# Optimization experiments

Measured on AMD Instinct MI355X. Metric: run time of the kernel, lower is better.

The kernel has to match this reference:

```python
import jax, jax.numpy as jnp
import numpy as np

B, ACT, C, H = 2048, 14, 128, 32
N = B * ACT                      # total nodes
E = B * ACT * ACT                # batched GCN edges
LOG_STD_MIN, LOG_STD_MAX = -20.0, 2.0


def setup_inputs() -> dict:
    key = jax.random.key(0)
    ks = jax.random.split(key, 8)
    def w(k, shape, fan_in):
        return jax.random.normal(k, shape, jnp.float32) / np.sqrt(fan_in).astype(np.float32)
    return {
        "state": jax.random.normal(ks[0], (N, C), jnp.float32),
        "conv_W": w(ks[1], (C, C), C),
        "conv_b": jnp.zeros((C,), jnp.float32),
        "lin1_W": w(ks[2], (2 * C, H), 2 * C),
        "lin1_b": jnp.zeros((H,), jnp.float32),
        "lin2_W": w(ks[3], (H, H), H),
        "lin2_b": jnp.zeros((H,), jnp.float32),
        "mu_W": w(ks[4], (H, 1), H),
        "mu_b": jnp.zeros((1,), jnp.float32),
        "sig_W": w(ks[5], (H, 1), H),
        "sig_b": jnp.zeros((1,), jnp.float32),
        "edge_index": jax.random.randint(ks[6], (2, E), 0, N, jnp.int32),
    }


def gcn_conv(x, W, b, src, dst):
    # PyG GCNConv default: add self-loops + symmetric normalization
    xw = x @ W                                           # [N, C]
    ones = jnp.ones(src.shape, x.dtype)
    deg = jax.ops.segment_sum(ones, dst, num_segments=N) + 1.0   # self-loop included
    dinv = jax.lax.rsqrt(deg)                            # deg^{-1/2}
    norm = dinv[src] * dinv[dst]                         # per-edge weight
    agg = jax.ops.segment_sum(xw[src] * norm[:, None], dst, num_segments=N)
    return agg + xw * (dinv * dinv)[:, None] + b         # self-loop term + bias


def reference(state, conv_W, conv_b, lin1_W, lin1_b, lin2_W, lin2_b,
              mu_W, mu_b, sig_W, sig_b, edge_index):
    src, dst = edge_index[0], edge_index[1]
    out = jax.nn.relu(gcn_conv(state, conv_W, conv_b, src, dst))
    x = (out + state).reshape(B, ACT, C)                 # [B, 14, C]
    # self.edges = all 196 directed pairs (i, j) over the 14-node graph
    e_src = jnp.repeat(jnp.arange(ACT), ACT)             # edges[:, 0]
    e_dst = jnp.tile(jnp.arange(ACT), ACT)               # edges[:, 1]
    ef = jnp.concatenate([x[:, e_src, :], x[:, e_dst, :]], axis=2)  # [B, 196, 2C]
    h = jax.nn.leaky_relu(ef @ lin1_W + lin1_b)          # slope 0.01 (torch default)
    h = jax.nn.leaky_relu(h @ lin2_W + lin2_b)           # [B, 196, H]
    log_std = jnp.clip(h @ sig_W + sig_b, LOG_STD_MIN, LOG_STD_MAX)
    std = jnp.exp(log_std)[..., 0]                       # [B, 196]
    mu = jax.nn.softplus(h @ mu_W + mu_b + 1e-10)[..., 0]  # [B, 196]
    # distribution parameters (return_D / deterministic paths)
    return jnp.stack([mu, std], axis=0)                  # [2, B, 196]
```

## Files before the change

### kernel.cpp

```cpp
#include <hip/hip_runtime.h>
#include <hip/hip_bf16.h>
#include <math.h>

#define NB    2048
#define ACT   14
#define NC    128
#define NH    32
#define NNODE (NB*ACT)
#define NEDGE (NB*ACT*ACT)
#define NPAIR (NB*ACT*ACT)
#define BCAP  64

typedef __attribute__((ext_vector_type(8))) short bf16x8;
typedef __attribute__((ext_vector_type(4))) float f32x4;

__device__ __forceinline__ unsigned short f2bf(float f)
{
    unsigned u = __float_as_uint(f);
    return (unsigned short)((u + 0x7fff + ((u >> 16) & 1)) >> 16);
}
__device__ __forceinline__ float bf2f(unsigned short h)
{
    return __uint_as_float(((unsigned)h) << 16);
}
__device__ __forceinline__ float bfl(unsigned v) { return __uint_as_float(v << 16); }
__device__ __forceinline__ float bfh(unsigned v) { return __uint_as_float(v & 0xffff0000u); }

__global__ __launch_bounds__(256) void init_misc(
    int* __restrict__ cnt, unsigned short* __restrict__ ydummy,
    const float* __restrict__ convW, unsigned short* __restrict__ convWt,
    const float* __restrict__ W1,
    unsigned short* __restrict__ Whi, unsigned short* __restrict__ Wlo)
{
    int idx = blockIdx.x * 256 + threadIdx.x;
    if (idx < NNODE) cnt[idx] = 0;
    if (idx < 128) ydummy[idx] = 0;
    if (idx < 128 * 128) {
        int c = idx >> 7, k = idx & 127;
        convWt[idx] = f2bf(convW[k * 128 + c]);
    }
    if (idx < 64 * 128) {
        int c = idx >> 7, k = idx & 127;
        float w = (c < 32) ? W1[k * 32 + c] : W1[(128 + k) * 32 + (c - 32)];
        unsigned short h = f2bf(w);
        Whi[idx] = h;
        Wlo[idx] = f2bf(w - bf2f(h));
    }
}

__global__ void bucket_fill(const int* __restrict__ src, const int* __restrict__ dst,
                            int* __restrict__ cnt, int* __restrict__ bucket)
{
    int e = blockIdx.x * blockDim.x + threadIdx.x;
    if (e < NEDGE) {
        int d = dst[e];
        int slot = atomicAdd(&cnt[d], 1);
        if (slot < BCAP) bucket[(size_t)d * BCAP + slot] = src[e];
    }
}

__global__ __launch_bounds__(256) void gemm1_mfma(
    const float* __restrict__ A, const unsigned short* __restrict__ Bt,
    const int* __restrict__ cnt, unsigned short* __restrict__ y)
{
    __shared__ unsigned short Ah[128 * 128];
    __shared__ unsigned short Alo[128 * 128];
    __shared__ unsigned short Bl[128 * 128];
    const int tid  = threadIdx.x;
    const int row0 = blockIdx.x * 128;

#pragma unroll
    for (int it = 0; it < 16; ++it) {
        int idx = tid + it * 256;
        int r = idx >> 5;
        int c = (idx & 31) << 2;
        float4 v = ((const float4*)(A + (size_t)(row0 + r) * 128))[idx & 31];
        ushort4 h, l;
        h.x = f2bf(v.x); l.x = f2bf(v.x - bf2f(h.x));
        h.y = f2bf(v.y); l.y = f2bf(v.y - bf2f(h.y));
        h.z = f2bf(v.z); l.z = f2bf(v.z - bf2f(h.z));
        h.w = f2bf(v.w); l.w = f2bf(v.w - bf2f(h.w));
        int byte = (r * 256 + c * 2) ^ ((r & 7) << 4);
        *(ushort4*)((char*)Ah  + byte) = h;
        *(ushort4*)((char*)Alo + byte) = l;
    }
#pragma unroll
    for (int it = 0; it < 8; ++it) {
        int idx = tid + it * 256;
        int cc = idx >> 4;
        int kk = (idx & 15) << 3;
        bf16x8 v = *((const bf16x8*)(Bt + cc * 128 + kk));
        int byte = (cc * 256 + kk * 2) ^ ((cc & 7) << 4);
        *(bf16x8*)((char*)Bl + byte) = v;
    }
    __syncthreads();

    const int wv = tid >> 6, lane = tid & 63;
    const int lr = lane & 15, kb = lane >> 4;
    const int col0 = wv * 32;

    f32x4 acc0[8], acc1[8];
#pragma unroll
    for (int mt = 0; mt < 8; ++mt) {
        acc0[mt] = (f32x4){0.f, 0.f, 0.f, 0.f};
        acc1[mt] = (f32x4){0.f, 0.f, 0.f, 0.f};
    }

#pragma unroll
    for (int ks = 0; ks < 4; ++ks) {
        const int kbyte = (ks * 32 + kb * 8) * 2;
        int cb0 = ((col0 + lr) * 256 + kbyte) ^ (((col0 + lr) & 7) << 4);
        int cb1 = ((col0 + 16 + lr) * 256 + kbyte) ^ (((col0 + 16 + lr) & 7) << 4);
        bf16x8 b0 = *(const bf16x8*)((char*)Bl + cb0);
        bf16x8 b1 = *(const bf16x8*)((char*)Bl + cb1);
#pragma unroll
        for (int mt = 0; mt < 8; ++mt) {
            int rr = mt * 16 + lr;
            int ab = (rr * 256 + kbyte) ^ ((rr & 7) << 4);
            bf16x8 ah = *(const bf16x8*)((char*)Ah  + ab);
            bf16x8 al = *(const bf16x8*)((char*)Alo + ab);
            acc0[mt] = __builtin_amdgcn_mfma_f32_16x16x32_bf16(ah, b0, acc0[mt], 0, 0, 0);
            acc0[mt] = __builtin_amdgcn_mfma_f32_16x16x32_bf16(al, b0, acc0[mt], 0, 0, 0);
            acc1[mt] = __builtin_amdgcn_mfma_f32_16x16x32_bf16(ah, b1, acc1[mt], 0, 0, 0);
            acc1[mt] = __builtin_amdgcn_mfma_f32_16x16x32_bf16(al, b1, acc1[mt], 0, 0, 0);
        }
    }

#pragma unroll
    for (int mt = 0; mt < 8; ++mt) {
#pragma unroll
        for (int t = 0; t < 4; ++t) {
            int grow = row0 + mt * 16 + kb * 4 + t;
            float s = rsqrtf((float)cnt[grow] + 1.0f);
            y[(size_t)grow * 128 + col0 + lr]      = f2bf(acc0[mt][t] * s);
            y[(size_t)grow * 128 + col0 + 16 + lr] = f2bf(acc1[mt][t] * s);
        }
    }
}

__global__ __launch_bounds__(256) void gemm2_mfma(
    const float* __restrict__ X, const unsigned short* __restrict__ Whi,
    const unsigned short* __restrict__ Wlo, float* __restrict__ U)
{
    __shared__ unsigned short Ah[64 * 128];
    __shared__ unsigned short Alo[64 * 128];
    __shared__ unsigned short Bh[64 * 128];
    __shared__ unsigned short Blo[64 * 128];
    const int tid  = threadIdx.x;
    const int row0 = blockIdx.x * 64;

#pragma unroll
    for (int it = 0; it < 8; ++it) {
        int idx = tid + it * 256;
        int r = idx >> 5;
        int c = (idx & 31) << 2;
        float4 v = ((const float4*)(X + (size_t)(row0 + r) * 128))[idx & 31];
        ushort4 h, l;
        h.x = f2bf(v.x); l.x = f2bf(v.x - bf2f(h.x));
        h.y = f2bf(v.y); l.y = f2bf(v.y - bf2f(h.y));
        h.z = f2bf(v.z); l.z = f2bf(v.z - bf2f(h.z));
        h.w = f2bf(v.w); l.w = f2bf(v.w - bf2f(h.w));
        int byte = (r * 256 + c * 2) ^ ((r & 7) << 4);
        *(ushort4*)((char*)Ah  + byte) = h;
        *(ushort4*)((char*)Alo + byte) = l;
    }
#pragma unroll
    for (int it = 0; it < 4; ++it) {
        int idx = tid + it * 256;
        int cc = idx >> 4;
        int kk = (idx & 15) << 3;
        int byte = (cc * 256 + kk * 2) ^ ((cc & 7) << 4);
        *(bf16x8*)((char*)Bh  + byte) = *((const bf16x8*)(Whi + cc * 128 + kk));
        *(bf16x8*)((char*)Blo + byte) = *((const bf16x8*)(Wlo + cc * 128 + kk));
    }
    __syncthreads();

    const int wv = tid >> 6, lane = tid & 63;
    const int lr = lane & 15, kb = lane >> 4;
    const int col0 = wv * 16;

    f32x4 acc[4];
#pragma unroll
    for (int mt = 0; mt < 4; ++mt) acc[mt] = (f32x4){0.f, 0.f, 0.f, 0.f};

#pragma unroll
    for (int ks = 0; ks < 4; ++ks) {
        const int kbyte = (ks * 32 + kb * 8) * 2;
        int cb = ((col0 + lr) * 256 + kbyte) ^ (((col0 + lr) & 7) << 4);
        bf16x8 bh = *(const bf16x8*)((char*)Bh  + cb);
        bf16x8 bl = *(const bf16x8*)((char*)Blo + cb);
#pragma unroll
        for (int mt = 0; mt < 4; ++mt) {
            int rr = mt * 16 + lr;
            int ab = (rr * 256 + kbyte) ^ ((rr & 7) << 4);
            bf16x8 ah = *(const bf16x8*)((char*)Ah  + ab);
            bf16x8 al = *(const bf16x8*)((char*)Alo + ab);
            acc[mt] = __builtin_amdgcn_mfma_f32_16x16x32_bf16(ah, bh, acc[mt], 0, 0, 0);
            acc[mt] = __builtin_amdgcn_mfma_f32_16x16x32_bf16(al, bh, acc[mt], 0, 0, 0);
            acc[mt] = __builtin_amdgcn_mfma_f32_16x16x32_bf16(ah, bl, acc[mt], 0, 0, 0);
        }
    }

#pragma unroll
    for (int mt = 0; mt < 4; ++mt) {
#pragma unroll
        for (int t = 0; t < 4; ++t) {
            int grow = row0 + mt * 16 + kb * 4 + t;
            U[(size_t)grow * 64 + col0 + lr] = acc[mt][t];
        }
    }
}

__global__ __launch_bounds__(256) void gather_agg(
    const int* __restrict__ bucket, const int* __restrict__ cnt,
    const unsigned short* __restrict__ y, const float* __restrict__ bias,
    const float* __restrict__ state, float* __restrict__ xout)
{
    const int lane = threadIdx.x & 31;
    const int d = (blockIdx.x * 256 + threadIdx.x) >> 5;
    if (d >= NNODE) return;

    const int c_true = cnt[d];
    const int c = c_true < BCAP ? c_true : BCAP;

    uint2 sv0 = ((const uint2*)(y + (size_t)d * NC))[lane];
    float4 acc;
    acc.x = bfl(sv0.x); acc.y = bfh(sv0.x);
    acc.z = bfl(sv0.y); acc.w = bfh(sv0.y);

    const int* brow = bucket + (size_t)d * BCAP;
    for (int base = 0; base < c; base += 32) {
        int rem = c - base;
        int m = rem < 32 ? rem : 32;
        int sv = (lane < m) ? brow[base + lane] : NNODE;
        int mm = (m + 3) & ~3;
        for (int j = 0; j < mm; j += 4) {
            int s0 = __shfl(sv, j + 0, 32);
            int s1 = __shfl(sv, j + 1, 32);
            int s2 = __shfl(sv, j + 2, 32);
            int s3 = __shfl(sv, j + 3, 32);
            uint2 a0 = ((const uint2*)(y + (size_t)s0 * NC))[lane];
            uint2 a1 = ((const uint2*)(y + (size_t)s1 * NC))[lane];
            uint2 a2 = ((const uint2*)(y + (size_t)s2 * NC))[lane];
            uint2 a3 = ((const uint2*)(y + (size_t)s3 * NC))[lane];
            acc.x += bfl(a0.x) + bfl(a1.x) + bfl(a2.x) + bfl(a3.x);
            acc.y += bfh(a0.x) + bfh(a1.x) + bfh(a2.x) + bfh(a3.x);
            acc.z += bfl(a0.y) + bfl(a1.y) + bfl(a2.y) + bfl(a3.y);
            acc.w += bfh(a0.y) + bfh(a1.y) + bfh(a2.y) + bfh(a3.y);
        }
    }

    const float dv = rsqrtf((float)c_true + 1.0f);
    float4 b  = ((const float4*)bias)[lane];
    float4 st = ((const float4*)(state + (size_t)d * NC))[lane];
    float4 r;
    r.x = fmaxf(acc.x * dv + b.x, 0.f) + st.x;
    r.y = fmaxf(acc.y * dv + b.y, 0.f) + st.y;
    r.z = fmaxf(acc.z * dv + b.z, 0.f) + st.z;
    r.w = fmaxf(acc.w * dv + b.w, 0.f) + st.w;
    ((float4*)(xout + (size_t)d * NC))[lane] = r;
}

__device__ __forceinline__ float softplusf(float z)
{
    return z > 0.f ? z + log1pf(expf(-z)) : log1pf(expf(z));
}

__global__ __launch_bounds__(256) void pairs_lds_kernel(
    const float* __restrict__ uv, const float* __restrict__ W2,
    const float* __restrict__ b1, const float* __restrict__ b2,
    const float* __restrict__ muW, const float* __restrict__ mu_b,
    const float* __restrict__ sigW, const float* __restrict__ sig_b,
    float* __restrict__ out)
{
    __shared__ float uvs[42 * 68];
    const int tid = threadIdx.x;
    const int b0 = (blockIdx.x * 256) / 196;
    const int nodebase = b0 * ACT;

#pragma unroll
    for (int it = 0; it < 3; ++it) {
        int c = tid + it * 256;
        if (c < 42 * 16) {
            int r = c >> 4, q = c & 15;
            if (nodebase + r < NNODE) {
                float4 v = ((const float4*)(uv + (size_t)(nodebase + r) * 64))[q];
                *((float4*)&uvs[r * 68 + q * 4]) = v;
            }
        }
    }
    __syncthreads();

    const int gid = blockIdx.x * 256 + tid;
    const int b = gid / 196;
    const int p = gid - b * 196;
    const int i = p / 14;
    const int j = p - i * 14;

    const float* up = uvs + ((b - b0) * ACT + i) * 68;
    const float* vp = uvs + ((b - b0) * ACT + j) * 68 + 32;

    float h2[32];
#pragma unroll
    for (int l = 0; l < 32; ++l) h2[l] = b2[l];

#pragma unroll 2
    for (int k4 = 0; k4 < 8; ++k4) {
        float4 uu = *((const float4*)(up + k4 * 4));
        float4 vv = *((const float4*)(vp + k4 * 4));
#pragma unroll
        for (int kk = 0; kk < 4; ++kk) {
            float uvk = (kk == 0) ? uu.x + vv.x :
                        (kk == 1) ? uu.y + vv.y :
                        (kk == 2) ? uu.z + vv.z : uu.w + vv.w;
            float z = uvk + b1[k4 * 4 + kk];
            float h1k = z > 0.f ? z : 0.01f * z;
            const float* wrow = W2 + (k4 * 4 + kk) * 32;
#pragma unroll
            for (int l = 0; l < 32; ++l)
                h2[l] += h1k * wrow[l];
        }
    }

    float mu_acc = mu_b[0] + 1e-10f;
    float sg = sig_b[0];
#pragma unroll
    for (int l = 0; l < 32; ++l) {
        float h = h2[l];
        h = h > 0.f ? h : 0.01f * h;
        mu_acc += h * muW[l];
        sg += h * sigW[l];
    }
    out[gid]         = softplusf(mu_acc);
    out[NPAIR + gid] = expf(fminf(fmaxf(sg, -20.f), 2.f));
}

extern "C" void kernel_launch(void* const* d_in, const int* in_sizes, int n_in,
                              void* d_out, int out_size, void* d_ws, size_t ws_size,
                              hipStream_t stream)
{
    const float* state  = (const float*)d_in[0];
    const float* conv_W = (const float*)d_in[1];
    const float* conv_b = (const float*)d_in[2];
    const float* lin1_W = (const float*)d_in[3];
    const float* lin1_b = (const float*)d_in[4];
    const float* lin2_W = (const float*)d_in[5];
    const float* lin2_b = (const float*)d_in[6];
    const float* mu_W   = (const float*)d_in[7];
    const float* mu_b   = (const float*)d_in[8];
    const float* sig_W  = (const float*)d_in[9];
    const float* sig_b  = (const float*)d_in[10];
    const int*   eidx   = (const int*)d_in[11];
    const int* e_src = eidx;
    const int* e_dst = eidx + NEDGE;

    float* out = (float*)d_out;

    char* wsb = (char*)d_ws;
    unsigned short* y = (unsigned short*)wsb;
    char* p = wsb + (size_t)(NNODE + 1) * NC * sizeof(unsigned short);
    float* x = (float*)p;            p += (size_t)NNODE * NC * sizeof(float);
    int* cnt = (int*)p;              p += (size_t)NNODE * sizeof(int);
    int* bucket = (int*)p;           p += (size_t)NNODE * BCAP * sizeof(int);
    unsigned short* convWt = (unsigned short*)p;  p += 128 * 128 * sizeof(unsigned short);
    unsigned short* Whi = (unsigned short*)p;     p += 64 * 128 * sizeof(unsigned short);
    unsigned short* Wlo = (unsigned short*)p;     p += 64 * 128 * sizeof(unsigned short);
    float* uvb = (float*)p;

    init_misc<<<(NNODE + 255) / 256, 256, 0, stream>>>(
        cnt, y + (size_t)NNODE * NC, conv_W, convWt, lin1_W, Whi, Wlo);

    bucket_fill<<<NEDGE / 256, 256, 0, stream>>>(e_src, e_dst, cnt, bucket);

    gemm1_mfma<<<NNODE / 128, 256, 0, stream>>>(state, convWt, cnt, y);

    gather_agg<<<(NNODE * 32) / 256, 256, 0, stream>>>(
        bucket, cnt, y, conv_b, state, x);

    gemm2_mfma<<<NNODE / 64, 256, 0, stream>>>(x, Whi, Wlo, uvb);

    pairs_lds_kernel<<<NPAIR / 256, 256, 0, stream>>>(
        uvb, lin2_W, lin1_b, lin2_b, mu_W, mu_b, sig_W, sig_b, out);
}
```

Before: 83.00 us.

## Compute pair-MLP second layer with bf16 MFMA instead of scalar FMA

The per-pair 32x32 lin2 matmul, previously a scalar FMA loop per thread, now runs on the matrix cores via mfma_f32_16x16x32_bf16. lin2_W is pre-transposed into a bf16 column-major buffer during init, and each wave handles 4 tiles of 16 pairs. Results are staged through shared memory so each thread can finish the mu/sigma heads for its own pair. This cuts the large FMA count and register pressure, but adds bf16 rounding on h1 and W2, plus extra LDS traffic and shared memory per block.

Result: faster. 76.93 us (-7.3%).

```diff
diff --git a/kernel.cpp b/kernel.cpp
--- a/kernel.cpp
+++ b/kernel.cpp
@@ -30,7 +30,8 @@
     int* __restrict__ cnt, unsigned short* __restrict__ ydummy,
     const float* __restrict__ convW, unsigned short* __restrict__ convWt,
     const float* __restrict__ W1,
-    unsigned short* __restrict__ Whi, unsigned short* __restrict__ Wlo)
+    unsigned short* __restrict__ Whi, unsigned short* __restrict__ Wlo,
+    const float* __restrict__ W2, unsigned short* __restrict__ W2cm)
 {
     int idx = blockIdx.x * 256 + threadIdx.x;
     if (idx < NNODE) cnt[idx] = 0;
@@ -45,6 +46,10 @@
         unsigned short h = f2bf(w);
         Whi[idx] = h;
         Wlo[idx] = f2bf(w - bf2f(h));
+    }
+    if (idx < 1024) {
+        int c = idx >> 5, kk = idx & 31;
+        W2cm[c * 32 + kk] = f2bf(W2[kk * 32 + c]);
     }
 }
 
@@ -265,16 +270,26 @@
 {
     return z > 0.f ? z + log1pf(expf(-z)) : log1pf(expf(z));
 }
-
-__global__ __launch_bounds__(256) void pairs_lds_kernel(
-    const float* __restrict__ uv, const float* __restrict__ W2,
+__device__ __forceinline__ float leakyf(float z)
+{
+    return z > 0.f ? z : 0.01f * z;
+}
+
+__global__ __launch_bounds__(256) void pairs_mfma5_kernel(
+    const float* __restrict__ uv, const unsigned short* __restrict__ W2cm,
     const float* __restrict__ b1, const float* __restrict__ b2,
     const float* __restrict__ muW, const float* __restrict__ mu_b,
     const float* __restrict__ sigW, const float* __restrict__ sig_b,
     float* __restrict__ out)
 {
     __shared__ float uvs[42 * 68];
-    const int tid = threadIdx.x;
+    __shared__ float h2s[4][64 * 33];
+    const int tid  = threadIdx.x;
+    const int wv   = tid >> 6;
+    const int lane = tid & 63;
+    const int lr   = lane & 15;
+    const int kb   = lane >> 4;
+    const int k0   = kb * 8;
     const int b0 = (blockIdx.x * 256) / 196;
     const int nodebase = b0 * ACT;
 
@@ -289,50 +304,63 @@
             }
         }
     }
+    bf16x8 bfr0 = *((const bf16x8*)(W2cm + (size_t)lr * 32 + k0));
+    bf16x8 bfr1 = *((const bf16x8*)(W2cm + (size_t)(16 + lr) * 32 + k0));
+    float4 c0 = *((const float4*)(b1 + k0));
+    float4 c1 = *((const float4*)(b1 + k0 + 4));
     __syncthreads();
 
-    const int gid = blockIdx.x * 256 + tid;
-    const int b = gid / 196;
-    const int p = gid - b * 196;
-    const int i = p / 14;
-    const int j = p - i * 14;
-
-    const float* up = uvs + ((b - b0) * ACT + i) * 68;
-    const float* vp = uvs + ((b - b0) * ACT + j) * 68 + 32;
-
-    float h2[32];
-#pragma unroll
-    for (int l = 0; l < 32; ++l) h2[l] = b2[l];
-
-#pragma unroll 2
-    for (int k4 = 0; k4 < 8; ++k4) {
-        float4 uu = *((const float4*)(up + k4 * 4));
-        float4 vv = *((const float4*)(vp + k4 * 4));
-#pragma unroll
-        for (int kk = 0; kk < 4; ++kk) {
-            float uvk = (kk == 0) ? uu.x + vv.x :
-                        (kk == 1) ? uu.y + vv.y :
-                        (kk == 2) ? uu.z + vv.z : uu.w + vv.w;
-            float z = uvk + b1[k4 * 4 + kk];
-            float h1k = z > 0.f ? z : 0.01f * z;
-            const float* wrow = W2 + (k4 * 4 + kk) * 32;
-#pragma unroll
-            for (int l = 0; l < 32; ++l)
-                h2[l] += h1k * wrow[l];
+    float* h2w = h2s[wv];
+#pragma unroll
+    for (int tt = 0; tt < 4; ++tt) {
+        const int g = blockIdx.x * 256 + wv * 64 + tt * 16 + lr;
+        const int b = g / 196;
+        const int p = g - b * 196;
+        const int i = p / 14;
+        const int j = p - i * 14;
+        const float* up = &uvs[((b - b0) * ACT + i) * 68 + k0];
+        const float* vp = &uvs[((b - b0) * ACT + j) * 68 + 32 + k0];
+        float4 u0 = *((const float4*)up);
+        float4 u1 = *((const float4*)(up + 4));
+        float4 v0 = *((const float4*)vp);
+        float4 v1 = *((const float4*)(vp + 4));
+
+        bf16x8 a;
+        a[0] = (short)f2bf(leakyf(u0.x + v0.x + c0.x));
+        a[1] = (short)f2bf(leakyf(u0.y + v0.y + c0.y));
+        a[2] = (short)f2bf(leakyf(u0.z + v0.z + c0.z));
+        a[3] = (short)f2bf(leakyf(u0.w + v0.w + c0.w));
+        a[4] = (short)f2bf(leakyf(u1.x + v1.x + c1.x));
+        a[5] = (short)f2bf(leakyf(u1.y + v1.y + c1.y));
+        a[6] = (short)f2bf(leakyf(u1.z + v1.z + c1.z));
+        a[7] = (short)f2bf(leakyf(u1.w + v1.w + c1.w));
+
+        f32x4 A0 = {0.f, 0.f, 0.f, 0.f};
+        f32x4 A1 = {0.f, 0.f, 0.f, 0.f};
+        A0 = __builtin_amdgcn_mfma_f32_16x16x32_bf16(a, bfr0, A0, 0, 0, 0);
+        A1 = __builtin_amdgcn_mfma_f32_16x16x32_bf16(a, bfr1, A1, 0, 0, 0);
+
+        const int rowb = tt * 16 + kb * 4;
+#pragma unroll
+        for (int t = 0; t < 4; ++t) {
+            h2w[(rowb + t) * 33 + lr]      = A0[t];
+            h2w[(rowb + t) * 33 + 16 + lr] = A1[t];
         }
     }
 
     float mu_acc = mu_b[0] + 1e-10f;
     float sg = sig_b[0];
+    const float* myrow = &h2w[lane * 33];
 #pragma unroll
     for (int l = 0; l < 32; ++l) {
-        float h = h2[l];
+        float h = myrow[l] + b2[l];
         h = h > 0.f ? h : 0.01f * h;
         mu_acc += h * muW[l];
-        sg += h * sigW[l];
-    }
-    out[gid]         = softplusf(mu_acc);
-    out[NPAIR + gid] = expf(fminf(fmaxf(sg, -20.f), 2.f));
+        sg     += h * sigW[l];
+    }
+    const int g2 = blockIdx.x * 256 + wv * 64 + lane;
+    out[g2]         = softplusf(mu_acc);
+    out[NPAIR + g2] = expf(fminf(fmaxf(sg, -20.f), 2.f));
 }
 
 extern "C" void kernel_launch(void* const* d_in, const int* in_sizes, int n_in,
@@ -365,10 +393,12 @@
     unsigned short* convWt = (unsigned short*)p;  p += 128 * 128 * sizeof(unsigned short);
     unsigned short* Whi = (unsigned short*)p;     p += 64 * 128 * sizeof(unsigned short);
     unsigned short* Wlo = (unsigned short*)p;     p += 64 * 128 * sizeof(unsigned short);
+    unsigned short* W2cm = (unsigned short*)p;    p += 1024 * sizeof(unsigned short);
     float* uvb = (float*)p;
 
     init_misc<<<(NNODE + 255) / 256, 256, 0, stream>>>(
-        cnt, y + (size_t)NNODE * NC, conv_W, convWt, lin1_W, Whi, Wlo);
+        cnt, y + (size_t)NNODE * NC, conv_W, convWt, lin1_W, Whi, Wlo,
+        lin2_W, W2cm);
 
     bucket_fill<<<NEDGE / 256, 256, 0, stream>>>(e_src, e_dst, cnt, bucket);
 
@@ -379,6 +409,6 @@
 
     gemm2_mfma<<<NNODE / 64, 256, 0, stream>>>(x, Whi, Wlo, uvb);
 
-    pairs_lds_kernel<<<NPAIR / 256, 256, 0, stream>>>(
-        uvb, lin2_W, lin1_b, lin2_b, mu_W, mu_b, sig_W, sig_b, out);
-}
+    pairs_mfma5_kernel<<<NPAIR / 256, 256, 0, stream>>>(
+        uvb, W2cm, lin1_b, lin2_b, mu_W, mu_b, sig_W, sig_b, out);
+}
```
